# Optimization experiments

Hardware: AMD Instinct MI355X
Metric: run time of the kernel (lower is better)

The kernel has to match this reference:

```python
import jax, jax.numpy as jnp
import numpy as np

D = 2048
NH = 16
DH = D // NH            # 128
DHR = DH // 2           # 64
DC = D // 2             # 1024
DCQ = D // 2            # 1024
B, L = 4, 2048
ROPE_BASE = 10000.0


def setup_inputs() -> dict:
    key = jax.random.key(0)
    ks = jax.random.split(key, 10)
    s = 0.02
    inp = {
        "x": jax.random.normal(ks[0], (B, L, D), dtype=jnp.float32),
        "W_DKV": jax.random.normal(ks[1], (D, DC), dtype=jnp.float32) * s,
        "W_UK": jax.random.normal(ks[2], (DC, NH * DH), dtype=jnp.float32) * s,
        "W_UV": jax.random.normal(ks[3], (DC, NH * DH), dtype=jnp.float32) * s,
        "W_DQ": jax.random.normal(ks[4], (D, DCQ), dtype=jnp.float32) * s,
        "W_UQ": jax.random.normal(ks[5], (DCQ, NH * DH), dtype=jnp.float32) * s,
        "W_QR": jax.random.normal(ks[6], (DCQ, NH * DHR), dtype=jnp.float32) * s,
        "W_KR": jax.random.normal(ks[7], (D, DHR), dtype=jnp.float32) * s,
        "W_O": jax.random.normal(ks[8], (D, D), dtype=jnp.float32) * s,
        "s_qk": jnp.asarray(np.sqrt(DH + DHR), dtype=jnp.float32),
    }
    return inp


def _rope_tables(seq_len, dim, dtype):
    # Standard rotate-half RoPE tables: cos/sin of shape (seq_len, dim)
    inv_freq = 1.0 / (ROPE_BASE ** (jnp.arange(0, dim, 2, dtype=jnp.float32) / dim))
    t = jnp.arange(seq_len, dtype=jnp.float32)
    freqs = jnp.outer(t, inv_freq)            # (L, dim/2)
    emb = jnp.concatenate([freqs, freqs], axis=-1)  # (L, dim)
    return jnp.cos(emb).astype(dtype), jnp.sin(emb).astype(dtype)


def _apply_rope(x, cos, sin):
    # x: (B, H, L, dim); cos/sin: (L, dim)
    half = x.shape[-1] // 2
    rot = jnp.concatenate([-x[..., half:], x[..., :half]], axis=-1)
    return x * cos[None, None] + rot * sin[None, None]


def reference(x, W_DKV, W_UK, W_UV, W_DQ, W_UQ, W_QR, W_KR, W_O, s_qk):
    Bb, Ll, Dd = x.shape
    cos, sin = _rope_tables(Ll, DHR, x.dtype)

    c_kv = x @ W_DKV                                            # (B,L,DC)
    k_c = (c_kv @ W_UK).reshape(Bb, Ll, NH, DH).transpose(0, 2, 1, 3)
    v = (c_kv @ W_UV).reshape(Bb, Ll, NH, DH).transpose(0, 2, 1, 3)

    c_q = x @ W_DQ                                              # (B,L,DCQ)
    q_c = (c_q @ W_UQ).reshape(Bb, Ll, NH, DH).transpose(0, 2, 1, 3)
    q_rope = _apply_rope((c_q @ W_QR).reshape(Bb, Ll, NH, DHR).transpose(0, 2, 1, 3), cos, sin)
    k_rope = _apply_rope((x @ W_KR).reshape(Bb, Ll, 1, DHR).transpose(0, 2, 1, 3), cos, sin)
    k_rope = jnp.broadcast_to(k_rope, (Bb, NH, Ll, DHR))

    q = jnp.concatenate([q_c, q_rope], axis=-1)                 # (B,H,L,DH+DHR)
    k = jnp.concatenate([k_c, k_rope], axis=-1)

    eps = 1e-12
    q = q / jnp.maximum(jnp.linalg.norm(q, axis=-1, keepdims=True), eps)
    k = k / jnp.maximum(jnp.linalg.norm(k, axis=-1, keepdims=True), eps)

    # SDPA with scale=1.0, causal mask, q pre-scaled by s_qk
    scores = jnp.einsum("bhqd,bhkd->bhqk", q * s_qk, k)         # (B,H,L,L)
    causal = jnp.tril(jnp.ones((Ll, Ll), dtype=bool))
    scores = jnp.where(causal[None, None], scores, jnp.finfo(scores.dtype).min)
    attn = jax.nn.softmax(scores, axis=-1)
    out = jnp.einsum("bhqk,bhkd->bhqd", attn, v)                # (B,H,L,DH)
    out = out.transpose(0, 2, 1, 3).reshape(Bb, Ll, Dd)
    return out @ W_O
```

## Files before the change

### kernel.cpp

```cpp
#include <hip/hip_runtime.h>
#include <stdint.h>

typedef unsigned short u16;
typedef unsigned int u32;
typedef short bf16x8 __attribute__((ext_vector_type(8)));
typedef float f32x4 __attribute__((ext_vector_type(4)));
typedef u16 u16x4 __attribute__((ext_vector_type(4)));

#define DEV __device__ __forceinline__

DEV float bf2f(u16 u) { union { float f; u32 i; } x; x.i = ((u32)u) << 16; return x.f; }
DEV u16 f2bf(float f) {
  union { float f; u32 i; } x; x.f = f;
  u32 i = x.i;
  u32 r = (i + 0x7fffu + ((i >> 16) & 1u)) >> 16;
  return (u16)r;
}

DEV void gl_lds16(const u16* g, u16* l) {
  __builtin_amdgcn_global_load_lds((const __attribute__((address_space(1))) u32*)g,
                                   (__attribute__((address_space(3))) u32*)l, 16, 0, 0);
}

__global__ __launch_bounds__(256) void prep(const float* __restrict__ x,
                                            const float* __restrict__ W_DKV,
                                            const float* __restrict__ W_UK,
                                            const float* __restrict__ W_UV,
                                            const float* __restrict__ W_DQ,
                                            const float* __restrict__ W_UQ,
                                            const float* __restrict__ W_QR,
                                            const float* __restrict__ W_KR,
                                            const float* __restrict__ W_O,
                                            u16* __restrict__ xb,
                                            u16* __restrict__ WtDKVQ,
                                            u16* __restrict__ WtUKV,
                                            u16* __restrict__ WtKR,
                                            u16* __restrict__ WtO) {
  __shared__ float tile[64][65];
  const int tid = threadIdx.x;
  int bid = blockIdx.x;

  if (bid < 4096) {
#pragma unroll
    for (int it = 0; it < 4; ++it) {
      int i = bid * 1024 + it * 256 + tid;
      float4 v = ((const float4*)x)[i];
      u16x4 o;
      o.x = f2bf(v.x); o.y = f2bf(v.y); o.z = f2bf(v.z); o.w = f2bf(v.w);
      ((u16x4*)xb)[i] = o;
    }
    return;
  }
  bid -= 4096;

  const float* W; u16* Wt; int K, N;
  if (bid < 512)        { W = W_DKV; Wt = WtDKVQ;                K = 2048; N = 1024; }
  else if (bid < 1024)  { W = W_DQ;  Wt = WtDKVQ + 1024 * 2048;  K = 2048; N = 1024; bid -= 512; }
  else if (bid < 1536)  { W = W_UK;  Wt = WtUKV;                 K = 1024; N = 2048; bid -= 1024; }
  else if (bid < 2048)  { W = W_UV;  Wt = WtUKV + 2048 * 1024;   K = 1024; N = 2048; bid -= 1536; }
  else if (bid < 2560)  { W = W_UQ;  Wt = WtUKV + 4096 * 1024;   K = 1024; N = 2048; bid -= 2048; }
  else if (bid < 2816)  { W = W_QR;  Wt = WtUKV + 6144 * 1024;   K = 1024; N = 1024; bid -= 2560; }
  else if (bid < 2848)  { W = W_KR;  Wt = WtKR;                  K = 2048; N = 64;   bid -= 2816; }
  else                  { W = W_O;   Wt = WtO;                   K = 2048; N = 2048; bid -= 2848; }

  const int gx = N >> 6;
  const int n0 = (bid % gx) * 64;
  const int k0 = (bid / gx) * 64;
#pragma unroll
  for (int i = 0; i < 16; ++i) {
    int idx = tid + i * 256;
    int r = idx >> 6, c = idx & 63;
    tile[r][c] = W[(size_t)(k0 + r) * N + n0 + c];
  }
  __syncthreads();
#pragma unroll
  for (int i = 0; i < 16; ++i) {
    int idx = tid + i * 256;
    int r = idx >> 6, c = idx & 63;
    Wt[(size_t)(n0 + r) * K + k0 + c] = f2bf(tile[c][r]);
  }
}

DEV void ep_set(u16* E, int i, float v) { E[i] = f2bf(v); }
DEV void ep_set(float* E, int i, float v) { E[i] = v; }

template <typename OT, int KIND>
__global__ __launch_bounds__(512, 2) void gemm256(const u16* __restrict__ A, int lda,
                                                  const u16* __restrict__ Bt,
                                                  OT* __restrict__ C, int ldc, int K,
                                                  u16* __restrict__ X1, u16* __restrict__ X2,
                                                  const u16* __restrict__ A2,
                                                  const u16* __restrict__ B2,
                                                  u16* __restrict__ C2) {
  __shared__ u16 smem[65536];
  const int tid = threadIdx.x;
  const int lane = tid & 63;
  const int w = tid >> 6;
  const int wm = w >> 2;
  const int wn = w & 3;
  const int quad = lane >> 4;
  const int l15 = lane & 15;
  const int cs = quad ^ ((l15 >> 1) & 3);

  int m0, n0;
  if constexpr (KIND == 2) {
    const int lin2 = blockIdx.x;
    if (lin2 < 32) {
      const int idx = lin2;
      u16* Ab2 = smem;
      u16* Bb2 = smem + 32768;
      const u16* Ag2 = A2 + (size_t)(idx * 256) * 2048;
      auto stg = [&](int t2, int bufi) {
        u16* Ad = Ab2 + bufi * 16384;
        u16* Bd = Bb2 + bufi * 4096;
#pragma unroll
        for (int i = 0; i < 4; ++i) {
          int cb = i * 512 + w * 64;
          int c = cb + lane;
          int r = c >> 3, cp = (c & 7) ^ (r & 7);
          gl_lds16(Ag2 + (size_t)r * 2048 + t2 * 64 + cp * 8, &Ad[cb * 8]);
        }
        {
          int cb = w * 64;
          int c = cb + lane;
          int r = c >> 3, cp = (c & 7) ^ (r & 7);
          gl_lds16(B2 + (size_t)r * 2048 + t2 * 64 + cp * 8, &Bd[cb * 8]);
        }
      };
      f32x4 acc2[2][4] = {};
      stg(0, 0);
      __syncthreads();
      for (int t2 = 0; t2 < 32; ++t2) {
        int cur = t2 & 1;
        if (t2 + 1 < 32) stg(t2 + 1, cur ^ 1);
        const u16* Ad = Ab2 + cur * 16384;
        const u16* Bd = Bb2 + cur * 4096;
#pragma unroll
        for (int kq = 0; kq < 2; ++kq) {
          bf16x8 bfr[4];
#pragma unroll
          for (int n = 0; n < 4; ++n)
            bfr[n] = *(const bf16x8*)&Bd[(n * 16 + l15) * 64 + ((kq * 4 + quad) ^ (l15 & 7)) * 8];
#pragma unroll
          for (int mt = 0; mt < 2; ++mt) {
            bf16x8 afr = *(const bf16x8*)&Ad[(w * 32 + mt * 16 + l15) * 64 + ((kq * 4 + quad) ^ (l15 & 7)) * 8];
#pragma unroll
            for (int n = 0; n < 4; ++n)
              acc2[mt][n] = __builtin_amdgcn_mfma_f32_16x16x32_bf16(afr, bfr[n], acc2[mt][n], 0, 0, 0);
          }
        }
        __syncthreads();
      }
#pragma unroll
      for (int mt = 0; mt < 2; ++mt)
#pragma unroll
        for (int n = 0; n < 4; ++n)
#pragma unroll
          for (int r = 0; r < 4; ++r)
            C2[(size_t)(idx * 256 + w * 32 + mt * 16 + quad * 4 + r) * 64 + n * 16 + l15] =
                f2bf(acc2[mt][n][r]);
      return;
    }
    const int c = lin2 - 32;
    const int cc = (c & 7) * 112 + (c >> 3);
    const int g4 = cc >> 2;
    n0 = (g4 % 28) * 256;
    m0 = ((g4 / 28) * 4 + (cc & 3)) * 256;
  } else {
    const int nwg = gridDim.x * gridDim.y;
    const int lin = blockIdx.y * gridDim.x + blockIdx.x;
    const int swz = (lin & 7) * (nwg >> 3) + (lin >> 3);
    const int g4 = swz >> 2;
    n0 = (g4 % gridDim.x) * 256;
    m0 = ((g4 / gridDim.x) * 4 + (swz & 3)) * 256;
  }

  const int rloc = tid >> 2;
  const int clog = (tid & 3) ^ ((tid >> 3) & 3);
  const u16* Abase = A + ((KIND == 2 && n0 >= 4096) ? 1024 : 0);
  const size_t aoff0 = (size_t)rloc * lda + clog * 8;
  const size_t boff0 = (size_t)rloc * (size_t)K + clog * 8;
  const u16* Ag = Abase + (size_t)m0 * lda;
  const u16* Bg = Bt + (size_t)n0 * K;

  auto stageA = [&](int u, int ks2) {
    u16* dst = smem + (u & 1) * 32768 + ks2 * 8192 + w * 512;
    const u16* s0 = Ag + aoff0 + u * 64 + ks2 * 32;
    gl_lds16(s0, dst);
    gl_lds16(s0 + (size_t)128 * lda, dst + 4096);
  };
  auto stageB = [&](int u, int ks2) {
    u16* dst = smem + (u & 1) * 32768 + 16384 + ks2 * 8192 + w * 512;
    const u16* s0 = Bg + boff0 + u * 64 + ks2 * 32;
    gl_lds16(s0, dst);
    gl_lds16(s0 + (size_t)128 * (size_t)K, dst + 4096);
  };

  f32x4 acc[2][4][4] = {};
  const int nt = K >> 6;

  stageA(0, 0); stageB(0, 0); stageA(0, 1); stageB(0, 1);
  stageA(1, 0); stageB(1, 0);
  asm volatile("s_waitcnt vmcnt(4)" ::: "memory");
  __builtin_amdgcn_s_barrier();

  for (int t = 0; t < nt; ++t) {
    const u16* As_ = smem + (t & 1) * 32768;
    const u16* Bs_ = As_ + 16384;
#pragma unroll
    for (int p = 0; p < 4; ++p) {
      const int ks = p >> 1;
      const int mq = p & 1;
      const u16* Ab = As_ + ks * 8192;
      const u16* Bb = Bs_ + ks * 8192;
      bf16x8 af[4], bf[4];
#pragma unroll
      for (int mt = 0; mt < 4; ++mt)
        af[mt] = *(const bf16x8*)&Ab[(wm * 128 + mq * 64 + mt * 16 + l15) * 32 + cs * 8];
#pragma unroll
      for (int n = 0; n < 4; ++n)
        bf[n] = *(const bf16x8*)&Bb[(wn * 64 + n * 16 + l15) * 32 + cs * 8];
      if (p == 0)      { if (t + 1 < nt) stageA(t + 1, 1); }
      else if (p == 1) { if (t + 1 < nt) stageB(t + 1, 1); }
      else if (p == 2) { if (t + 2 < nt) stageA(t + 2, 0); }
      else             { if (t + 2 < nt) stageB(t + 2, 0); }
      __builtin_amdgcn_s_barrier();
      __builtin_amdgcn_s_setprio(1);
#pragma unroll
      for (int mt = 0; mt < 4; ++mt)
#pragma unroll
        for (int n = 0; n < 4; ++n)
          acc[mq][mt][n] = __builtin_amdgcn_mfma_f32_16x16x32_bf16(af[mt], bf[n], acc[mq][mt][n], 0, 0, 0);
      __builtin_amdgcn_s_setprio(0);
      if (p == 3) asm volatile("s_waitcnt vmcnt(4)" ::: "memory");
      __builtin_amdgcn_s_barrier();
    }
  }
  asm volatile("s_waitcnt vmcnt(0)" ::: "memory");
  __builtin_amdgcn_s_barrier();

  if constexpr (KIND == 2) {
    if (n0 >= 2048 && n0 < 4096) {
      u16* Ewt = smem + w * 2560;
      const int dvb = (n0 - 2048) + wn * 64;
      const int hh = dvb >> 7;
      const int dv0 = dvb & 127;
#pragma unroll
      for (int mq = 0; mq < 2; ++mq)
#pragma unroll
        for (int mh = 0; mh < 2; ++mh) {
#pragma unroll
          for (int mi = 0; mi < 2; ++mi)
#pragma unroll
            for (int n = 0; n < 4; ++n)
#pragma unroll
              for (int r = 0; r < 4; ++r)
                Ewt[(n * 16 + l15) * 40 + mi * 16 + quad * 4 + r] = f2bf(acc[mq][mh * 2 + mi][n][r]);
          asm volatile("s_waitcnt lgkmcnt(0)" ::: "memory");
          const int mbase = m0 + wm * 128 + mq * 64 + mh * 32;
          const int b_ = mbase >> 11, l_ = mbase & 2047;
          u16* dstp = X1 + ((size_t)((b_ * 16 + hh) * 128 + dv0 + lane)) * 2048 + l_;
          const u16* srcp = &Ewt[lane * 40];
#pragma unroll
          for (int k2 = 0; k2 < 4; ++k2)
            *(uint4*)&dstp[k2 * 8] = *(const uint4*)&srcp[k2 * 8];
          asm volatile("s_waitcnt lgkmcnt(0)" ::: "memory");
        }
      return;
    }
  }

  OT* Cc = C; int ldcc = ldc, col0 = n0;
  if constexpr (KIND == 2) {
    if (n0 >= 4096) { Cc = (OT*)X2; ldcc = 3072; col0 = n0 - 4096; }
  }
  OT* Ew = ((OT*)smem) + w * 1024;
#pragma unroll
  for (int mq = 0; mq < 2; ++mq) {
#pragma unroll
    for (int mt = 0; mt < 4; ++mt) {
#pragma unroll
      for (int n = 0; n < 4; ++n)
#pragma unroll
        for (int r = 0; r < 4; ++r)
          ep_set(Ew, (quad * 4 + r) * 64 + n * 16 + l15, acc[mq][mt][n][r]);
      asm volatile("s_waitcnt lgkmcnt(0)" ::: "memory");
#pragma unroll
      for (int it2 = 0; it2 < 4; ++it2) {
        int row_i = it2 * 4 + quad;
        size_t off = (size_t)(m0 + wm * 128 + mq * 64 + mt * 16 + row_i) * ldcc + col0 + wn * 64 + l15 * 4;
        if constexpr (sizeof(OT) == 2) {
          *(u16x4*)&Cc[off] = *(const u16x4*)&Ew[row_i * 64 + l15 * 4];
        } else {
          *(float4*)&Cc[off] = *(const float4*)&Ew[row_i * 64 + l15 * 4];
        }
      }
      asm volatile("s_waitcnt lgkmcnt(0)" ::: "memory");
    }
  }
}

__global__ __launch_bounds__(256) void build_k(const u16* __restrict__ kc,
                                               const u16* __restrict__ krr,
                                               u16* __restrict__ kn) {
  const int wid = blockIdx.x * 4 + (threadIdx.x >> 6);
  const int lane = threadIdx.x & 63;
  const int token = wid >> 4;
  const int h = wid & 15;
  const int b = token >> 11;
  const int l = token & 2047;
  float v0 = bf2f(kc[(size_t)token * 2048 + h * 128 + lane]);
  float v1 = bf2f(kc[(size_t)token * 2048 + h * 128 + 64 + lane]);
  int j = lane & 31;
  float freq = __expf((float)j * -0.28782313662425574f);
  float ang = (float)l * freq;
  float cs = __cosf(ang), sn = __sinf(ang);
  float xr = bf2f(krr[(size_t)token * 64 + lane]);
  float xo = bf2f(krr[(size_t)token * 64 + (lane ^ 32)]);
  float v2 = (lane < 32) ? (xr * cs - xo * sn) : (xr * cs + xo * sn);
  float ss = v0 * v0 + v1 * v1 + v2 * v2;
#pragma unroll
  for (int off = 1; off < 64; off <<= 1) ss += __shfl_xor(ss, off, 64);
  float scale = 1.0f / fmaxf(sqrtf(ss), 1e-12f);
  u16* out = kn + (((size_t)(b * 16 + h) * 2048) + l) * 192;
  out[lane] = f2bf(v0 * scale);
  out[64 + lane] = f2bf(v1 * scale);
  out[128 + lane] = f2bf(v2 * scale);
}

__global__ __launch_bounds__(512, 2) void flash_attn(const u16* __restrict__ qcr,
                                                     const u16* __restrict__ Kn,
                                                     const u16* __restrict__ Vt,
                                                     const float* __restrict__ s_qk,
                                                     u16* __restrict__ O) {
  constexpr int L = 2048, DQK = 192, KVB = 64;
  constexpr int PSTR = 72;
  __shared__ u16 smem[59392];
  u16* KsBuf = smem;
  u16* VsBuf = smem + 24576;
  u16* Ps    = smem + 40960;
  const int tid = threadIdx.x;
  const int lane = tid & 63;
  const int w = tid >> 6;
  const int quad = lane >> 4;
  const int l15 = lane & 15;
  const int lin = blockIdx.x;
  const int xcd = lin & 7;
  const int g = lin >> 3;
  const int bh = ((g >> 2) << 3) | xcd;
  const int pairIdx = g & 3;
  const int b = bh >> 4, h = bh & 15;
  const float SMAX = s_qk[0];

  const u16* Kg = Kn + (size_t)bh * L * DQK;
  const u16* Vg = Vt + (size_t)bh * 128 * L;

  int koffs[3], kdsts[3], voffs[2], vdsts[2];
#pragma unroll
  for (int it = 0; it < 3; ++it) {
    int p = it * 512 + w * 64 + lane;
    int r = p / 24, cp = p % 24;
    koffs[it] = r * DQK + (cp ^ (r & 7)) * 8;
    kdsts[it] = (it * 512 + w * 64) * 8;
  }
#pragma unroll
  for (int it = 0; it < 2; ++it) {
    int q = (it + 3) * 512 + w * 64 + lane - 1536;
    int dv = q >> 3, cp = q & 7;
    voffs[it] = dv * L + (cp ^ (dv & 7)) * 8;
    vdsts[it] = ((it + 3) * 512 + w * 64 - 1536) * 8;
  }

  auto stage = [&](int kt2, int bufi) {
    u16* KsB = KsBuf + bufi * 12288;
    u16* VsB = VsBuf + bufi * 8192;
    const u16* Kt = Kg + (size_t)(kt2 * KVB) * DQK;
    const u16* Vtb = Vg + kt2 * KVB;
#pragma unroll
    for (int it = 0; it < 3; ++it) gl_lds16(Kt + koffs[it], &KsB[kdsts[it]]);
#pragma unroll
    for (int it = 0; it < 2; ++it) gl_lds16(Vtb + voffs[it], &VsB[vdsts[it]]);
  };

  bf16x8 ones;
#pragma unroll
  for (int j = 0; j < 8; ++j) ones[j] = (short)0x3F80;

  for (int qp = 0; qp < 2; ++qp) {
    const int qt = (qp == 0) ? (7 - pairIdx) : pairIdx;

    bf16x8 qf[2][6];
#pragma unroll
    for (int mt = 0; mt < 2; ++mt) {
      const int row = qt * 256 + w * 32 + mt * 16 + l15;
      const u16* qr_ = qcr + (size_t)(b * 2048 + row) * 3072;
#pragma unroll
      for (int kd = 0; kd < 4; ++kd)
        qf[mt][kd] = *(const bf16x8*)&qr_[h * 128 + kd * 32 + quad * 8];
      bf16x8 a4 = *(const bf16x8*)&qr_[2048 + h * 64 + quad * 8];
      bf16x8 a5 = *(const bf16x8*)&qr_[2048 + h * 64 + 32 + quad * 8];
      float v4[8], v5[8];
      float ss = 0.f;
#pragma unroll
      for (int e = 0; e < 8; ++e) {
        int j = quad * 8 + e;
        float fr = __expf((float)j * -0.28782313662425574f);
        float ang = (float)row * fr;
        float cs2 = __cosf(ang), sn2 = __sinf(ang);
        float x4 = bf2f((u16)a4[e]), x5 = bf2f((u16)a5[e]);
        v4[e] = x4 * cs2 - x5 * sn2;
        v5[e] = x5 * cs2 + x4 * sn2;
        ss += v4[e] * v4[e] + v5[e] * v5[e];
      }
#pragma unroll
      for (int kd = 0; kd < 4; ++kd)
#pragma unroll
        for (int e = 0; e < 8; ++e) { float xv = bf2f((u16)qf[mt][kd][e]); ss += xv * xv; }
      ss += __shfl_xor(ss, 16, 64);
      ss += __shfl_xor(ss, 32, 64);
      float scale = SMAX / fmaxf(sqrtf(ss), 1e-12f);
#pragma unroll
      for (int kd = 0; kd < 4; ++kd) {
        bf16x8 t = qf[mt][kd];
#pragma unroll
        for (int e = 0; e < 8; ++e) t[e] = (short)f2bf(bf2f((u16)t[e]) * scale);
        qf[mt][kd] = t;
      }
      bf16x8 t4, t5;
#pragma unroll
      for (int e = 0; e < 8; ++e) { t4[e] = (short)f2bf(v4[e] * scale); t5[e] = (short)f2bf(v5[e] * scale); }
      qf[mt][4] = t4; qf[mt][5] = t5;
    }

    f32x4 oacc[2][8] = {};
    f32x4 accL[2] = {};

    const int nkv = 4 * (qt + 1);
    stage(0, 0);
    __syncthreads();

    for (int kt = 0; kt < nkv; ++kt) {
      const int cur = kt & 1;
      if (kt + 1 < nkv) stage(kt + 1, cur ^ 1);
      const u16* KsC = KsBuf + cur * 12288;
      const u16* VsC = VsBuf + cur * 8192;

      f32x4 s[2][4] = {};
      __builtin_amdgcn_s_setprio(1);
#pragma unroll
      for (int kd = 0; kd < 6; ++kd) {
#pragma unroll
        for (int nt = 0; nt < 4; ++nt) {
          int row = nt * 16 + l15;
          int cp = (kd * 4 + quad) ^ (l15 & 7);
          bf16x8 bb = *(const bf16x8*)&KsC[row * DQK + cp * 8];
#pragma unroll
          for (int mt = 0; mt < 2; ++mt)
            s[mt][nt] = __builtin_amdgcn_mfma_f32_16x16x32_bf16(qf[mt][kd], bb, s[mt][nt], 0, 0, 0);
        }
      }
      __builtin_amdgcn_s_setprio(0);

      const int kbase = kt * KVB;
      const bool nomask = (kbase + KVB - 1) <= (qt * 256 + w * 32);
      const int kcol0 = kbase + l15;
      u16* Pw = &Ps[w * 32 * PSTR];
#pragma unroll
      for (int mt = 0; mt < 2; ++mt) {
        const int qrow_base = qt * 256 + w * 32 + mt * 16 + quad * 4;
#pragma unroll
        for (int r = 0; r < 4; ++r)
#pragma unroll
          for (int nt = 0; nt < 4; ++nt) {
            float sv = s[mt][nt][r];
            if (!nomask && (kcol0 + nt * 16 > qrow_base + r)) sv = -1e30f;
            Pw[(mt * 16 + quad * 4 + r) * PSTR + nt * 16 + l15] = f2bf(__expf(sv - SMAX));
          }
      }
      asm volatile("s_waitcnt lgkmcnt(0)" ::: "memory");

      __builtin_amdgcn_s_setprio(1);
      bf16x8 pf[2][2];
#pragma unroll
      for (int mt = 0; mt < 2; ++mt)
#pragma unroll
        for (int kc2 = 0; kc2 < 2; ++kc2) {
          pf[mt][kc2] = *(const bf16x8*)&Pw[(mt * 16 + l15) * PSTR + kc2 * 32 + quad * 8];
          accL[mt] = __builtin_amdgcn_mfma_f32_16x16x32_bf16(pf[mt][kc2], ones, accL[mt], 0, 0, 0);
        }
#pragma unroll
      for (int nt2 = 0; nt2 < 8; ++nt2) {
        const int dv = nt2 * 16 + l15;
#pragma unroll
        for (int kc2 = 0; kc2 < 2; ++kc2) {
          int lc = (kc2 * 4 + quad) ^ (l15 & 7);
          bf16x8 vv = *(const bf16x8*)&VsC[dv * KVB + lc * 8];
#pragma unroll
          for (int mt = 0; mt < 2; ++mt)
            oacc[mt][nt2] = __builtin_amdgcn_mfma_f32_16x16x32_bf16(pf[mt][kc2], vv, oacc[mt][nt2], 0, 0, 0);
        }
      }
      __builtin_amdgcn_s_setprio(0);
      __syncthreads();
    }

    float rinv[2][4];
#pragma unroll
    for (int mt = 0; mt < 2; ++mt)
#pragma unroll
      for (int r = 0; r < 4; ++r) rinv[mt][r] = 1.0f / accL[mt][r];
    u16* Ew = smem + w * 2048;
#pragma unroll
    for (int mt = 0; mt < 2; ++mt) {
#pragma unroll
      for (int nt2 = 0; nt2 < 8; ++nt2)
#pragma unroll
        for (int r = 0; r < 4; ++r)
          Ew[(quad * 4 + r) * 128 + nt2 * 16 + l15] = f2bf(oacc[mt][nt2][r] * rinv[mt][r]);
      asm volatile("s_waitcnt lgkmcnt(0)" ::: "memory");
#pragma unroll
      for (int it2 = 0; it2 < 4; ++it2) {
        int row_i = it2 * 4 + quad;
        int lg = qt * 256 + w * 32 + mt * 16 + row_i;
        uint4 v = *(const uint4*)&Ew[row_i * 128 + l15 * 8];
        *(uint4*)&O[((size_t)b * L + lg) * 2048 + h * 128 + l15 * 8] = v;
      }
      asm volatile("s_waitcnt lgkmcnt(0)" ::: "memory");
    }
    __syncthreads();
  }
}

extern "C" void kernel_launch(void* const* d_in, const int* in_sizes, int n_in,
                              void* d_out, int out_size, void* d_ws, size_t ws_size,
                              hipStream_t stream) {
  const float* x     = (const float*)d_in[0];
  const float* W_DKV = (const float*)d_in[1];
  const float* W_UK  = (const float*)d_in[2];
  const float* W_UV  = (const float*)d_in[3];
  const float* W_DQ  = (const float*)d_in[4];
  const float* W_UQ  = (const float*)d_in[5];
  const float* W_QR  = (const float*)d_in[6];
  const float* W_KR  = (const float*)d_in[7];
  const float* W_O   = (const float*)d_in[8];
  const float* s_qk  = (const float*)d_in[9];

  char* base = (char*)d_ws;
  u16* xb     = (u16*)(base);
  u16* WtDKVQ = (u16*)(base + (size_t)33554432);
  u16* WtUKV  = (u16*)(base + (size_t)42991616);
  u16* WtO    = (u16*)(base + (size_t)57671680);
  u16* ckvq   = (u16*)(base + (size_t)66060288);
  u16* kc     = (u16*)(base + (size_t)99614720);
  u16* Vt     = (u16*)(base + (size_t)133169152);
  u16* qcr    = (u16*)(base + (size_t)166723584);
  u16* kr     = (u16*)(base + (size_t)217055232);
  u16* WtKR   = (u16*)(base + (size_t)218103808);
  u16* kn = (u16*)(base);
  u16* O  = ckvq;

  prep<<<7968, 256, 0, stream>>>(x, W_DKV, W_UK, W_UV, W_DQ, W_UQ, W_QR, W_KR, W_O,
                                 xb, WtDKVQ, WtUKV, WtKR, WtO);

  gemm256<u16, 0><<<dim3(8, 32), 512, 0, stream>>>(xb, 2048, WtDKVQ, ckvq, 2048, 2048,
                                                   nullptr, nullptr, nullptr, nullptr, nullptr);

  gemm256<u16, 2><<<dim3(928), 512, 0, stream>>>(ckvq, 2048, WtUKV, kc, 2048, 1024,
                                                 Vt, qcr, xb, WtKR, kr);

  build_k<<<32768, 256, 0, stream>>>(kc, kr, kn);

  flash_attn<<<dim3(256), 512, 0, stream>>>(qcr, kn, Vt, s_qk, O);

  gemm256<float, 0><<<dim3(8, 32), 512, 0, stream>>>(O, 2048, WtO, (float*)d_out, 2048, 2048,
                                                     nullptr, nullptr, nullptr, nullptr, nullptr);
}
```

Before: 594.9 us.

## Split fused up-projection GEMM into lighter kernel with smaller LDS for higher occupancy

Moves the fused K/V/Q up-projection and k-rope GEMM out of the templated gemm256 into a dedicated kernel. The new kernel uses half the shared memory (K-step 32, simple double buffering) and launch bounds of 4 blocks per CU. The goal is more resident workgroups and latency hiding for the 928-block grid. In exchange it drops the deeper 4-phase pipelined staging schedule, giving more barriers per unit of work and possible register pressure at the tighter launch bound.

```diff
diff --git a/kernel.cpp b/kernel.cpp
--- a/kernel.cpp
+++ b/kernel.cpp
@@ -84,14 +84,10 @@
 DEV void ep_set(u16* E, int i, float v) { E[i] = f2bf(v); }
 DEV void ep_set(float* E, int i, float v) { E[i] = v; }
 
-template <typename OT, int KIND>
+template <typename OT>
 __global__ __launch_bounds__(512, 2) void gemm256(const u16* __restrict__ A, int lda,
                                                   const u16* __restrict__ Bt,
-                                                  OT* __restrict__ C, int ldc, int K,
-                                                  u16* __restrict__ X1, u16* __restrict__ X2,
-                                                  const u16* __restrict__ A2,
-                                                  const u16* __restrict__ B2,
-                                                  u16* __restrict__ C2) {
+                                                  OT* __restrict__ C, int ldc, int K) {
   __shared__ u16 smem[65536];
   const int tid = threadIdx.x;
   const int lane = tid & 63;
@@ -102,85 +98,18 @@
   const int l15 = lane & 15;
   const int cs = quad ^ ((l15 >> 1) & 3);
 
-  int m0, n0;
-  if constexpr (KIND == 2) {
-    const int lin2 = blockIdx.x;
-    if (lin2 < 32) {
-      const int idx = lin2;
-      u16* Ab2 = smem;
-      u16* Bb2 = smem + 32768;
-      const u16* Ag2 = A2 + (size_t)(idx * 256) * 2048;
-      auto stg = [&](int t2, int bufi) {
-        u16* Ad = Ab2 + bufi * 16384;
-        u16* Bd = Bb2 + bufi * 4096;
-#pragma unroll
-        for (int i = 0; i < 4; ++i) {
-          int cb = i * 512 + w * 64;
-          int c = cb + lane;
-          int r = c >> 3, cp = (c & 7) ^ (r & 7);
-          gl_lds16(Ag2 + (size_t)r * 2048 + t2 * 64 + cp * 8, &Ad[cb * 8]);
-        }
-        {
-          int cb = w * 64;
-          int c = cb + lane;
-          int r = c >> 3, cp = (c & 7) ^ (r & 7);
-          gl_lds16(B2 + (size_t)r * 2048 + t2 * 64 + cp * 8, &Bd[cb * 8]);
-        }
-      };
-      f32x4 acc2[2][4] = {};
-      stg(0, 0);
-      __syncthreads();
-      for (int t2 = 0; t2 < 32; ++t2) {
-        int cur = t2 & 1;
-        if (t2 + 1 < 32) stg(t2 + 1, cur ^ 1);
-        const u16* Ad = Ab2 + cur * 16384;
-        const u16* Bd = Bb2 + cur * 4096;
-#pragma unroll
-        for (int kq = 0; kq < 2; ++kq) {
-          bf16x8 bfr[4];
-#pragma unroll
-          for (int n = 0; n < 4; ++n)
-            bfr[n] = *(const bf16x8*)&Bd[(n * 16 + l15) * 64 + ((kq * 4 + quad) ^ (l15 & 7)) * 8];
-#pragma unroll
-          for (int mt = 0; mt < 2; ++mt) {
-            bf16x8 afr = *(const bf16x8*)&Ad[(w * 32 + mt * 16 + l15) * 64 + ((kq * 4 + quad) ^ (l15 & 7)) * 8];
-#pragma unroll
-            for (int n = 0; n < 4; ++n)
-              acc2[mt][n] = __builtin_amdgcn_mfma_f32_16x16x32_bf16(afr, bfr[n], acc2[mt][n], 0, 0, 0);
-          }
-        }
-        __syncthreads();
-      }
-#pragma unroll
-      for (int mt = 0; mt < 2; ++mt)
-#pragma unroll
-        for (int n = 0; n < 4; ++n)
-#pragma unroll
-          for (int r = 0; r < 4; ++r)
-            C2[(size_t)(idx * 256 + w * 32 + mt * 16 + quad * 4 + r) * 64 + n * 16 + l15] =
-                f2bf(acc2[mt][n][r]);
-      return;
-    }
-    const int c = lin2 - 32;
-    const int cc = (c & 7) * 112 + (c >> 3);
-    const int g4 = cc >> 2;
-    n0 = (g4 % 28) * 256;
-    m0 = ((g4 / 28) * 4 + (cc & 3)) * 256;
-  } else {
-    const int nwg = gridDim.x * gridDim.y;
-    const int lin = blockIdx.y * gridDim.x + blockIdx.x;
-    const int swz = (lin & 7) * (nwg >> 3) + (lin >> 3);
-    const int g4 = swz >> 2;
-    n0 = (g4 % gridDim.x) * 256;
-    m0 = ((g4 / gridDim.x) * 4 + (swz & 3)) * 256;
-  }
+  const int nwg = gridDim.x * gridDim.y;
+  const int lin = blockIdx.y * gridDim.x + blockIdx.x;
+  const int swz = (lin & 7) * (nwg >> 3) + (lin >> 3);
+  const int g4 = swz >> 2;
+  const int n0 = (g4 % gridDim.x) * 256;
+  const int m0 = ((g4 / gridDim.x) * 4 + (swz & 3)) * 256;
 
   const int rloc = tid >> 2;
   const int clog = (tid & 3) ^ ((tid >> 3) & 3);
-  const u16* Abase = A + ((KIND == 2 && n0 >= 4096) ? 1024 : 0);
   const size_t aoff0 = (size_t)rloc * lda + clog * 8;
   const size_t boff0 = (size_t)rloc * (size_t)K + clog * 8;
-  const u16* Ag = Abase + (size_t)m0 * lda;
+  const u16* Ag = A + (size_t)m0 * lda;
   const u16* Bg = Bt + (size_t)n0 * K;
 
   auto stageA = [&](int u, int ks2) {
@@ -239,41 +168,6 @@
   asm volatile("s_waitcnt vmcnt(0)" ::: "memory");
   __builtin_amdgcn_s_barrier();
 
-  if constexpr (KIND == 2) {
-    if (n0 >= 2048 && n0 < 4096) {
-      u16* Ewt = smem + w * 2560;
-      const int dvb = (n0 - 2048) + wn * 64;
-      const int hh = dvb >> 7;
-      const int dv0 = dvb & 127;
-#pragma unroll
-      for (int mq = 0; mq < 2; ++mq)
-#pragma unroll
-        for (int mh = 0; mh < 2; ++mh) {
-#pragma unroll
-          for (int mi = 0; mi < 2; ++mi)
-#pragma unroll
-            for (int n = 0; n < 4; ++n)
-#pragma unroll
-              for (int r = 0; r < 4; ++r)
-                Ewt[(n * 16 + l15) * 40 + mi * 16 + quad * 4 + r] = f2bf(acc[mq][mh * 2 + mi][n][r]);
-          asm volatile("s_waitcnt lgkmcnt(0)" ::: "memory");
-          const int mbase = m0 + wm * 128 + mq * 64 + mh * 32;
-          const int b_ = mbase >> 11, l_ = mbase & 2047;
-          u16* dstp = X1 + ((size_t)((b_ * 16 + hh) * 128 + dv0 + lane)) * 2048 + l_;
-          const u16* srcp = &Ewt[lane * 40];
-#pragma unroll
-          for (int k2 = 0; k2 < 4; ++k2)
-            *(uint4*)&dstp[k2 * 8] = *(const uint4*)&srcp[k2 * 8];
-          asm volatile("s_waitcnt lgkmcnt(0)" ::: "memory");
-        }
-      return;
-    }
-  }
-
-  OT* Cc = C; int ldcc = ldc, col0 = n0;
-  if constexpr (KIND == 2) {
-    if (n0 >= 4096) { Cc = (OT*)X2; ldcc = 3072; col0 = n0 - 4096; }
-  }
   OT* Ew = ((OT*)smem) + w * 1024;
 #pragma unroll
   for (int mq = 0; mq < 2; ++mq) {
@@ -288,12 +182,196 @@
 #pragma unroll
       for (int it2 = 0; it2 < 4; ++it2) {
         int row_i = it2 * 4 + quad;
+        size_t off = (size_t)(m0 + wm * 128 + mq * 64 + mt * 16 + row_i) * ldc + n0 + wn * 64 + l15 * 4;
+        if constexpr (sizeof(OT) == 2) {
+          *(u16x4*)&C[off] = *(const u16x4*)&Ew[row_i * 64 + l15 * 4];
+        } else {
+          *(float4*)&C[off] = *(const float4*)&Ew[row_i * 64 + l15 * 4];
+        }
+      }
+      asm volatile("s_waitcnt lgkmcnt(0)" ::: "memory");
+    }
+  }
+}
+
+__global__ __launch_bounds__(512, 4) void g23_lite(const u16* __restrict__ A,
+                                                   const u16* __restrict__ Bt,
+                                                   u16* __restrict__ kc,
+                                                   u16* __restrict__ Vt,
+                                                   u16* __restrict__ qcr,
+                                                   const u16* __restrict__ A2,
+                                                   const u16* __restrict__ B2,
+                                                   u16* __restrict__ C2) {
+  __shared__ u16 smem[32768];
+  const int tid = threadIdx.x;
+  const int lane = tid & 63;
+  const int w = tid >> 6;
+  const int wm = w >> 2;
+  const int wn = w & 3;
+  const int quad = lane >> 4;
+  const int l15 = lane & 15;
+  const int cs = quad ^ ((l15 >> 1) & 3);
+  constexpr int K = 1024, lda = 2048;
+
+  const int lin2 = blockIdx.x;
+  if (lin2 < 32) {
+    const int idx = lin2;
+    u16* Ab2 = smem;
+    u16* Bb2 = smem + 16384;
+    const u16* Ag2 = A2 + (size_t)(idx * 256) * 2048;
+    auto stg = [&](int t2, int bufi) {
+      u16* Ad = Ab2 + bufi * 8192;
+      u16* Bd = Bb2 + bufi * 2048;
+#pragma unroll
+      for (int i = 0; i < 2; ++i) {
+        int cb = i * 512 + w * 64;
+        int ch = cb + lane;
+        int r = ch >> 2, cp = (ch & 3) ^ ((r >> 1) & 3);
+        gl_lds16(Ag2 + (size_t)r * 2048 + t2 * 32 + cp * 8, &Ad[cb * 8]);
+      }
+      if (w < 4) {
+        int cb = w * 64;
+        int ch = cb + lane;
+        int r = ch >> 2, cp = (ch & 3) ^ ((r >> 1) & 3);
+        gl_lds16(B2 + (size_t)r * 2048 + t2 * 32 + cp * 8, &Bd[cb * 8]);
+      }
+    };
+    f32x4 acc2[2][4] = {};
+    stg(0, 0);
+    __syncthreads();
+    for (int t2 = 0; t2 < 64; ++t2) {
+      int cur = t2 & 1;
+      if (t2 + 1 < 64) stg(t2 + 1, cur ^ 1);
+      const u16* Ad = Ab2 + cur * 8192;
+      const u16* Bd = Bb2 + cur * 2048;
+      bf16x8 bfr[4];
+#pragma unroll
+      for (int n = 0; n < 4; ++n)
+        bfr[n] = *(const bf16x8*)&Bd[(n * 16 + l15) * 32 + cs * 8];
+#pragma unroll
+      for (int mt = 0; mt < 2; ++mt) {
+        bf16x8 afr = *(const bf16x8*)&Ad[(w * 32 + mt * 16 + l15) * 32 + cs * 8];
+#pragma unroll
+        for (int n = 0; n < 4; ++n)
+          acc2[mt][n] = __builtin_amdgcn_mfma_f32_16x16x32_bf16(afr, bfr[n], acc2[mt][n], 0, 0, 0);
+      }
+      __syncthreads();
+    }
+#pragma unroll
+    for (int mt = 0; mt < 2; ++mt)
+#pragma unroll
+      for (int n = 0; n < 4; ++n)
+#pragma unroll
+        for (int r = 0; r < 4; ++r)
+          C2[(size_t)(idx * 256 + w * 32 + mt * 16 + quad * 4 + r) * 64 + n * 16 + l15] =
+              f2bf(acc2[mt][n][r]);
+    return;
+  }
+
+  const int c = lin2 - 32;
+  const int cc = (c & 7) * 112 + (c >> 3);
+  const int g4 = cc >> 2;
+  const int n0 = (g4 % 28) * 256;
+  const int m0 = ((g4 / 28) * 4 + (cc & 3)) * 256;
+
+  const int rloc = tid >> 2;
+  const int clog = (tid & 3) ^ ((tid >> 3) & 3);
+  const u16* Abase = A + ((n0 >= 4096) ? 1024 : 0);
+  const size_t aoff0 = (size_t)rloc * lda + clog * 8;
+  const size_t boff0 = (size_t)rloc * (size_t)K + clog * 8;
+  const u16* Ag = Abase + (size_t)m0 * lda;
+  const u16* Bg = Bt + (size_t)n0 * K;
+
+  auto stageA = [&](int u) {
+    u16* dst = smem + (u & 1) * 16384 + w * 512;
+    const u16* s0 = Ag + aoff0 + u * 32;
+    gl_lds16(s0, dst);
+    gl_lds16(s0 + (size_t)128 * lda, dst + 4096);
+  };
+  auto stageB = [&](int u) {
+    u16* dst = smem + (u & 1) * 16384 + 8192 + w * 512;
+    const u16* s0 = Bg + boff0 + u * 32;
+    gl_lds16(s0, dst);
+    gl_lds16(s0 + (size_t)128 * (size_t)K, dst + 4096);
+  };
+
+  f32x4 acc[2][4][4] = {};
+  constexpr int nt = K / 32;
+
+  stageA(0); stageB(0);
+  __syncthreads();
+
+  for (int u = 0; u < nt; ++u) {
+    const int cur = u & 1;
+    if (u + 1 < nt) { stageA(u + 1); stageB(u + 1); }
+    const u16* Ab = smem + cur * 16384;
+    const u16* Bb = Ab + 8192;
+    bf16x8 bf[4];
+#pragma unroll
+    for (int n = 0; n < 4; ++n)
+      bf[n] = *(const bf16x8*)&Bb[(wn * 64 + n * 16 + l15) * 32 + cs * 8];
+    __builtin_amdgcn_s_setprio(1);
+#pragma unroll
+    for (int mq = 0; mq < 2; ++mq) {
+#pragma unroll
+      for (int mt = 0; mt < 4; ++mt) {
+        bf16x8 af = *(const bf16x8*)&Ab[(wm * 128 + mq * 64 + mt * 16 + l15) * 32 + cs * 8];
+#pragma unroll
+        for (int n = 0; n < 4; ++n)
+          acc[mq][mt][n] = __builtin_amdgcn_mfma_f32_16x16x32_bf16(af, bf[n], acc[mq][mt][n], 0, 0, 0);
+      }
+    }
+    __builtin_amdgcn_s_setprio(0);
+    __syncthreads();
+  }
+
+  if (n0 >= 2048 && n0 < 4096) {
+    u16* Ewt = smem + w * 2560;
+    const int dvb = (n0 - 2048) + wn * 64;
+    const int hh = dvb >> 7;
+    const int dv0 = dvb & 127;
+#pragma unroll
+    for (int mq = 0; mq < 2; ++mq)
+#pragma unroll
+      for (int mh = 0; mh < 2; ++mh) {
+#pragma unroll
+        for (int mi = 0; mi < 2; ++mi)
+#pragma unroll
+          for (int n = 0; n < 4; ++n)
+#pragma unroll
+            for (int r = 0; r < 4; ++r)
+              Ewt[(n * 16 + l15) * 40 + mi * 16 + quad * 4 + r] = f2bf(acc[mq][mh * 2 + mi][n][r]);
+        asm volatile("s_waitcnt lgkmcnt(0)" ::: "memory");
+        const int mbase = m0 + wm * 128 + mq * 64 + mh * 32;
+        const int b_ = mbase >> 11, l_ = mbase & 2047;
+        u16* dstp = Vt + ((size_t)((b_ * 16 + hh) * 128 + dv0 + lane)) * 2048 + l_;
+        const u16* srcp = &Ewt[lane * 40];
+#pragma unroll
+        for (int k2 = 0; k2 < 4; ++k2)
+          *(uint4*)&dstp[k2 * 8] = *(const uint4*)&srcp[k2 * 8];
+        asm volatile("s_waitcnt lgkmcnt(0)" ::: "memory");
+      }
+    return;
+  }
+
+  u16* Cc = kc; int ldcc = 2048, col0 = n0;
+  if (n0 >= 4096) { Cc = qcr; ldcc = 3072; col0 = n0 - 4096; }
+  u16* Ew = smem + w * 1024;
+#pragma unroll
+  for (int mq = 0; mq < 2; ++mq) {
+#pragma unroll
+    for (int mt = 0; mt < 4; ++mt) {
+#pragma unroll
+      for (int n = 0; n < 4; ++n)
+#pragma unroll
+        for (int r = 0; r < 4; ++r)
+          Ew[(quad * 4 + r) * 64 + n * 16 + l15] = f2bf(acc[mq][mt][n][r]);
+      asm volatile("s_waitcnt lgkmcnt(0)" ::: "memory");
+#pragma unroll
+      for (int it2 = 0; it2 < 4; ++it2) {
+        int row_i = it2 * 4 + quad;
         size_t off = (size_t)(m0 + wm * 128 + mq * 64 + mt * 16 + row_i) * ldcc + col0 + wn * 64 + l15 * 4;
-        if constexpr (sizeof(OT) == 2) {
-          *(u16x4*)&Cc[off] = *(const u16x4*)&Ew[row_i * 64 + l15 * 4];
-        } else {
-          *(float4*)&Cc[off] = *(const float4*)&Ew[row_i * 64 + l15 * 4];
-        }
+        *(u16x4*)&Cc[off] = *(const u16x4*)&Ew[row_i * 64 + l15 * 4];
       }
       asm volatile("s_waitcnt lgkmcnt(0)" ::: "memory");
     }
@@ -562,16 +640,13 @@
   prep<<<7968, 256, 0, stream>>>(x, W_DKV, W_UK, W_UV, W_DQ, W_UQ, W_QR, W_KR, W_O,
                                  xb, WtDKVQ, WtUKV, WtKR, WtO);
 
-  gemm256<u16, 0><<<dim3(8, 32), 512, 0, stream>>>(xb, 2048, WtDKVQ, ckvq, 2048, 2048,
-                                                   nullptr, nullptr, nullptr, nullptr, nullptr);
-
-  gemm256<u16, 2><<<dim3(928), 512, 0, stream>>>(ckvq, 2048, WtUKV, kc, 2048, 1024,
-                                                 Vt, qcr, xb, WtKR, kr);
+  gemm256<u16><<<dim3(8, 32), 512, 0, stream>>>(xb, 2048, WtDKVQ, ckvq, 2048, 2048);
+
+  g23_lite<<<dim3(928), 512, 0, stream>>>(ckvq, WtUKV, kc, Vt, qcr, xb, WtKR, kr);
 
   build_k<<<32768, 256, 0, stream>>>(kc, kr, kn);
 
   flash_attn<<<dim3(256), 512, 0, stream>>>(qcr, kn, Vt, s_qk, O);
 
-  gemm256<float, 0><<<dim3(8, 32), 512, 0, stream>>>(O, 2048, WtO, (float*)d_out, 2048, 2048,
-                                                     nullptr, nullptr, nullptr, nullptr, nullptr);
-}
+  gemm256<float><<<dim3(8, 32), 512, 0, stream>>>(O, 2048, WtO, (float*)d_out, 2048, 2048);
+}
```

Result: slower. 1.227 ms (+106.3%).
